# Performance work log

Hardware: AMD Instinct MI355X
Metric: run time of the kernel (lower is better)

The kernel has to match this reference:

```python
import jax, jax.numpy as jnp
import numpy as np

B, M, K, L, E = 1024, 16, 32, 50, 64
NUM_ACT, NUM_USER = 100000, 500000
AVG_M = float(M)  # avg group size; equals M since groups are batched to fixed size


def setup_inputs() -> dict:
    key = jax.random.key(0)
    ks = jax.random.split(key, 24)
    s = 1.0 / np.sqrt(E)
    u = lambda k, shape: jax.random.uniform(k, shape, minval=-s, maxval=s, dtype=jnp.float32)
    return {
        "members": jax.random.randint(ks[0], (B, M), 0, NUM_USER),
        "neighbors": jax.random.randint(ks[1], (B, M, K), 0, NUM_USER),
        "act_inputs": jax.random.randint(ks[2], (B,), 0, NUM_ACT),
        "act_seqs": jax.random.randint(ks[3], (B, M, L), 0, NUM_ACT),
        "act_table": jax.random.normal(ks[4], (NUM_ACT, E), dtype=jnp.float32) * 0.02,
        "user_table": jax.random.normal(ks[5], (NUM_USER, E), dtype=jnp.float32) * 0.02,
        "W_ih": u(ks[6], (4 * E, E)),
        "W_hh": u(ks[7], (4 * E, E)),
        "b_ih": u(ks[8], (4 * E,)),
        "b_hh": u(ks[9], (4 * E,)),
        "gcn_W": u(ks[10], (E, E)),
        "gcn_b": u(ks[11], (E,)),
        "pna_W1": u(ks[12], (4 * E, E)),
        "pna_b1": u(ks[13], (E,)),
        "pna_W2": u(ks[14], (E, E)),
        "pna_b2": u(ks[15], (E,)),
        "pna_W3": u(ks[16], (E, E)),
        "pna_b3": u(ks[17], (E,)),
        "pred_W1": u(ks[18], (3 * E, 8)),
        "pred_b1": u(ks[19], (8,)),
        "pred_W2": u(ks[20], (8, 1)),
        "pred_b2": u(ks[21], (1,)),
    }


def _lstm_last(x, W_ih, W_hh, b):
    # x: [N, L, E]; returns last hidden state [N, E] (PyTorch gate order i,f,g,o)
    n = x.shape[0]
    h0 = jnp.zeros((n, E), x.dtype)

    def step(carry, xt):
        h, c = carry
        gates = xt @ W_ih.T + h @ W_hh.T + b  # [N, 4E]
        i, f, g, o = jnp.split(gates, 4, axis=-1)
        c = jax.nn.sigmoid(f) * c + jax.nn.sigmoid(i) * jnp.tanh(g)
        h = jax.nn.sigmoid(o) * jnp.tanh(c)
        return (h, c), None

    (h, _), _ = jax.lax.scan(step, (h0, h0), jnp.swapaxes(x, 0, 1))
    return h


def reference(members, neighbors, act_inputs, act_seqs, act_table, user_table,
              W_ih, W_hh, b_ih, b_hh, gcn_W, gcn_b,
              pna_W1, pna_b1, pna_W2, pna_b2, pna_W3, pna_b3,
              pred_W1, pred_b1, pred_W2, pred_b2):
    act_e = act_table[act_inputs]  # [B, E] target activity embeddings
    # per-member LSTM encoding of activity sequences, batched over all B*M members
    seq_e = act_table[act_seqs].reshape(B * M, L, E)
    m_act = _lstm_last(seq_e, W_ih, W_hh, b_ih + b_hh).reshape(B, M, E)
    # GCN: mean over {member} U neighbors, then linear + relu
    mem_e = user_table[members]                     # [B, M, E]
    nbr_sum = user_table[neighbors].sum(axis=2)     # [B, M, E]
    agg = (mem_e + nbr_sum) / (K + 1)
    m_gcn = jax.nn.relu(agg @ gcn_W.T + gcn_b)      # [B, M, E]
    fus = m_act + m_gcn                             # [B, M, E]
    # PNA-style set aggregation: {mean,max} x {identity, amplification}
    mean = fus.mean(axis=1)
    mx = fus.max(axis=1)
    amp = jnp.log(M + 1.0) / jnp.log(AVG_M + 1.0)
    feats = jnp.concatenate([mean, mx, mean * amp, mx * amp], axis=-1)  # [B, 4E]
    h = jax.nn.relu(feats @ pna_W1 + pna_b1)
    h = jax.nn.relu(h @ pna_W2 + pna_b2)
    grp = h @ pna_W3 + pna_b3                        # [B, E]
    # predict layer
    cat = jnp.concatenate([grp * act_e, grp, act_e], axis=-1)  # [B, 3E]
    hh = jax.nn.relu(cat @ pred_W1 + pred_b1)
    y = jax.nn.sigmoid(hh @ pred_W2 + pred_b2)       # [B, 1]
    return y
```

## Files before the change

kernel.cpp:

```cpp
#include <hip/hip_runtime.h>
#include <hip/hip_bf16.h>
#include <math.h>

#define BB   1024
#define MM   16
#define KK   32
#define LL   50
#define EE   64
#define NACT 100000

typedef __attribute__((ext_vector_type(8))) short short8;
typedef float v4f __attribute__((ext_vector_type(4)));

__device__ __forceinline__ float rcpf(float x) { return __builtin_amdgcn_rcpf(x); }
__device__ __forceinline__ float exp2_fast(float x) {
    float r;
    asm("v_exp_f32 %0, %1" : "=v"(r) : "v"(x));
    return r;
}

__device__ __forceinline__ unsigned cvt_pk_bf16(float lo, float hi) {
    unsigned r;
    asm("v_cvt_pk_bf16_f32 %0, %1, %2" : "=v"(r) : "v"(lo), "v"(hi));
    return r;
}

__device__ __forceinline__ void block_sync_lds() {
    __builtin_amdgcn_sched_barrier(0);
    asm volatile("s_waitcnt lgkmcnt(0)" ::: "memory");
    __builtin_amdgcn_s_barrier();
    __builtin_amdgcn_sched_barrier(0);
}

__global__ __launch_bounds__(256)
void cvt_table(const float* __restrict__ src, unsigned* __restrict__ dst)
{
    const int i = blockIdx.x * 256 + threadIdx.x;
    if (i < (NACT * EE) / 8) {
        const float4* s = reinterpret_cast<const float4*>(src) + (size_t)i * 2;
        float4 a = s[0], b = s[1];
        uint4 o;
        o.x = cvt_pk_bf16(a.x, a.y);
        o.y = cvt_pk_bf16(a.z, a.w);
        o.z = cvt_pk_bf16(b.x, b.y);
        o.w = cvt_pk_bf16(b.z, b.w);
        reinterpret_cast<uint4*>(dst)[i] = o;
    }
}

__global__ __launch_bounds__(256, 2)
void lstm_fused(const int* __restrict__ act_seqs, const unsigned short* __restrict__ act_bf,
                const int* __restrict__ members, const int* __restrict__ neighbors,
                const float* __restrict__ user_table,
                const float* __restrict__ W_ih, const float* __restrict__ W_hh,
                const float* __restrict__ b_ih, const float* __restrict__ b_hh,
                const int* __restrict__ act_inputs, const float* __restrict__ act_table,
                const float* __restrict__ gcn_W, const float* __restrict__ gcn_b,
                const float* __restrict__ pna_W1, const float* __restrict__ pna_b1,
                const float* __restrict__ pna_W2, const float* __restrict__ pna_b2,
                const float* __restrict__ pna_W3, const float* __restrict__ pna_b3,
                const float* __restrict__ pred_W1, const float* __restrict__ pred_b1,
                const float* __restrict__ pred_W2, const float* __restrict__ pred_b2,
                float* __restrict__ out)
{
    __shared__ __align__(16) short sH[4][1024];
    __shared__ int sIdx[32 * LL];
    __shared__ int sNbr[32 * 33];
    __shared__ float sFus[32][64];
    __shared__ float sAgg[32][64];
    __shared__ float sWg[64][66];
    __shared__ float sF[2][256];
    __shared__ float sP[2][2][64];
    __shared__ float sH1[2][64];
    __shared__ float sH2[2][64];
    __shared__ float sGrp[2][64];
    __shared__ float sActe[2][64];
    __shared__ float sHH[2][8];

    const int t    = threadIdx.x;
    const int blk  = blockIdx.x;
    const int lane = t & 63;
    const int w    = t >> 6;
    const int lr   = lane & 15;
    const int lb   = lane >> 4;

    for (int i = t; i < 32 * LL; i += 256) sIdx[i] = act_seqs[blk * (32 * LL) + i];
    for (int i = t; i < 32 * 33; i += 256) {
        const int p = i / 33, j = i - p * 33;
        const int base = blk * 32 + p;
        sNbr[i] = (j == 0) ? members[base] : neighbors[base * KK + j - 1];
    }

    const float L2E = 1.44269504088896f;
    float gscale[4];
    gscale[0] = -L2E; gscale[1] = -L2E; gscale[2] = 2.0f * L2E; gscale[3] = -L2E;

    short8 Bf[2][4][2];
    #pragma unroll
    for (int mat = 0; mat < 2; ++mat) {
        const float* W = mat ? W_hh : W_ih;
        #pragma unroll
        for (int g = 0; g < 4; ++g) {
            const int j = g * 64 + w * 16 + lr;
            const float sc = gscale[g];
            #pragma unroll
            for (int ks = 0; ks < 2; ++ks) {
                const float4* p = reinterpret_cast<const float4*>(&W[(size_t)j * 64 + ks * 32 + lb * 8]);
                float4 v0 = p[0], v1 = p[1];
                uint4 o;
                o.x = cvt_pk_bf16(sc * v0.x, sc * v0.y);
                o.y = cvt_pk_bf16(sc * v0.z, sc * v0.w);
                o.z = cvt_pk_bf16(sc * v1.x, sc * v1.y);
                o.w = cvt_pk_bf16(sc * v1.z, sc * v1.w);
                Bf[mat][g][ks] = __builtin_bit_cast(short8, o);
            }
        }
    }
    float bias[4];
    #pragma unroll
    for (int g = 0; g < 4; ++g) {
        const int j = g * 64 + w * 16 + lr;
        bias[g] = gscale[g] * (b_ih[j] + b_hh[j]);
    }

    float hA[4], cA[4], hB[4], cB[4];
    #pragma unroll
    for (int r = 0; r < 4; ++r) { hA[r] = 0.0f; cA[r] = 0.0f; hB[r] = 0.0f; cB[r] = 0.0f; }

    reinterpret_cast<uint4*>(sH)[t] = make_uint4(0u, 0u, 0u, 0u);
    __syncthreads();

    const int gpair = t >> 3;
    const int gec   = t & 7;
    const float* gut = user_table + (size_t)gec * 8;
    float gacc[8];
    #pragma unroll
    for (int q = 0; q < 8; ++q) gacc[q] = 0.0f;
    float4 gld0, gld1;
    {
        const int gi = sNbr[gpair * 33 + 0];
        const float4* gp = reinterpret_cast<const float4*>(gut + (size_t)gi * EE);
        gld0 = gp[0]; gld1 = gp[1];
    }

    const char* tbl8 = reinterpret_cast<const char*>(act_bf) + lb * 16;
    const int ibA = lr * LL;
    const int ibB = (16 + lr) * LL;

    int idA = sIdx[ibA + 0], idB = sIdx[ibB + 0];
    short8 axA0 = *reinterpret_cast<const short8*>(tbl8 + (size_t)idA * 128);
    short8 axA1 = *reinterpret_cast<const short8*>(tbl8 + (size_t)idA * 128 + 64);
    short8 axB0 = *reinterpret_cast<const short8*>(tbl8 + (size_t)idB * 128);
    short8 axB1 = *reinterpret_cast<const short8*>(tbl8 + (size_t)idB * 128 + 64);
    idA = sIdx[ibA + 1]; idB = sIdx[ibB + 1];

    const int offA0 = lr * 128 + ((lb ^ (lr & 7)) << 4);
    const int offA1 = lr * 128 + (((lb + 4) ^ (lr & 7)) << 4);
    int hw_off[4];
    #pragma unroll
    for (int r = 0; r < 4; ++r) {
        const int s = lb * 4 + r, e = w * 16 + lr;
        hw_off[r] = s * 128 + ((((e >> 3) ^ (s & 7)) << 4)) + (e & 7) * 2;
    }
    char* const sHb = reinterpret_cast<char*>(sH);

    #pragma unroll 2
    for (int step = 0; step < LL; ++step) {
        const int cb  = (step & 1) << 12;
        const int nb_ = cb ^ 4096;

        if (step < 33) {
            gacc[0] += gld0.x; gacc[1] += gld0.y; gacc[2] += gld0.z; gacc[3] += gld0.w;
            gacc[4] += gld1.x; gacc[5] += gld1.y; gacc[6] += gld1.z; gacc[7] += gld1.w;
            if (step < 32) {
                const int gi = sNbr[gpair * 33 + step + 1];
                const float4* gp = reinterpret_cast<const float4*>(gut + (size_t)gi * EE);
                gld0 = gp[0]; gld1 = gp[1];
            }
        }

        short8 nxA0 = *reinterpret_cast<const short8*>(tbl8 + (size_t)idA * 128);
        short8 nxA1 = *reinterpret_cast<const short8*>(tbl8 + (size_t)idA * 128 + 64);
        short8 nxB0 = *reinterpret_cast<const short8*>(tbl8 + (size_t)idB * 128);
        short8 nxB1 = *reinterpret_cast<const short8*>(tbl8 + (size_t)idB * 128 + 64);
        {
            const int s2 = (step + 2 < LL) ? (step + 2) : (LL - 1);
            idA = sIdx[ibA + s2]; idB = sIdx[ibB + s2];
        }

        short8 ahA0 = *reinterpret_cast<const short8*>(sHb + cb + offA0);
        short8 ahA1 = *reinterpret_cast<const short8*>(sHb + cb + offA1);
        short8 ahB0 = *reinterpret_cast<const short8*>(sHb + cb + 2048 + offA0);
        short8 ahB1 = *reinterpret_cast<const short8*>(sHb + cb + 2048 + offA1);

        v4f accA[4], accB[4];
        #pragma unroll
        for (int g = 0; g < 4; ++g) {
            v4f a; a[0] = bias[g]; a[1] = bias[g]; a[2] = bias[g]; a[3] = bias[g];
            accA[g] = a; accB[g] = a;
        }
        #pragma unroll
        for (int g = 0; g < 4; ++g) {
            accA[g] = __builtin_amdgcn_mfma_f32_16x16x32_bf16(axA0, Bf[0][g][0], accA[g], 0, 0, 0);
            accA[g] = __builtin_amdgcn_mfma_f32_16x16x32_bf16(axA1, Bf[0][g][1], accA[g], 0, 0, 0);
            accA[g] = __builtin_amdgcn_mfma_f32_16x16x32_bf16(ahA0, Bf[1][g][0], accA[g], 0, 0, 0);
            accA[g] = __builtin_amdgcn_mfma_f32_16x16x32_bf16(ahA1, Bf[1][g][1], accA[g], 0, 0, 0);
        }
        #pragma unroll
        for (int g = 0; g < 4; ++g) {
            accB[g] = __builtin_amdgcn_mfma_f32_16x16x32_bf16(axB0, Bf[0][g][0], accB[g], 0, 0, 0);
            accB[g] = __builtin_amdgcn_mfma_f32_16x16x32_bf16(axB1, Bf[0][g][1], accB[g], 0, 0, 0);
            accB[g] = __builtin_amdgcn_mfma_f32_16x16x32_bf16(ahB0, Bf[1][g][0], accB[g], 0, 0, 0);
            accB[g] = __builtin_amdgcn_mfma_f32_16x16x32_bf16(ahB1, Bf[1][g][1], accB[g], 0, 0, 0);
        }

        {
            char* SH = sHb + nb_;
            #pragma unroll
            for (int r = 0; r < 4; ++r) {
                const float si = rcpf(1.0f + exp2_fast(accA[0][r]));
                const float sf = rcpf(1.0f + exp2_fast(accA[1][r]));
                const float tg = fmaf(-2.0f, rcpf(1.0f + exp2_fast(accA[2][r])), 1.0f);
                const float so = rcpf(1.0f + exp2_fast(accA[3][r]));
                const float cc = fmaf(sf, cA[r], si * tg);
                cA[r] = cc;
                hA[r] = so * fmaf(-2.0f, rcpf(1.0f + exp2_fast(cc * (2.0f * L2E))), 1.0f);
            }
            const unsigned a01 = cvt_pk_bf16(hA[0], hA[1]);
            const unsigned a23 = cvt_pk_bf16(hA[2], hA[3]);
            *reinterpret_cast<short*>(SH + hw_off[0]) = (short)(a01 & 0xFFFF);
            *reinterpret_cast<short*>(SH + hw_off[1]) = (short)(a01 >> 16);
            *reinterpret_cast<short*>(SH + hw_off[2]) = (short)(a23 & 0xFFFF);
            *reinterpret_cast<short*>(SH + hw_off[3]) = (short)(a23 >> 16);
            SH += 2048;
            #pragma unroll
            for (int r = 0; r < 4; ++r) {
                const float si = rcpf(1.0f + exp2_fast(accB[0][r]));
                const float sf = rcpf(1.0f + exp2_fast(accB[1][r]));
                const float tg = fmaf(-2.0f, rcpf(1.0f + exp2_fast(accB[2][r])), 1.0f);
                const float so = rcpf(1.0f + exp2_fast(accB[3][r]));
                const float cc = fmaf(sf, cB[r], si * tg);
                cB[r] = cc;
                hB[r] = so * fmaf(-2.0f, rcpf(1.0f + exp2_fast(cc * (2.0f * L2E))), 1.0f);
            }
            const unsigned b01 = cvt_pk_bf16(hB[0], hB[1]);
            const unsigned b23 = cvt_pk_bf16(hB[2], hB[3]);
            *reinterpret_cast<short*>(SH + hw_off[0]) = (short)(b01 & 0xFFFF);
            *reinterpret_cast<short*>(SH + hw_off[1]) = (short)(b01 >> 16);
            *reinterpret_cast<short*>(SH + hw_off[2]) = (short)(b23 & 0xFFFF);
            *reinterpret_cast<short*>(SH + hw_off[3]) = (short)(b23 >> 16);
        }

        block_sync_lds();

        axA0 = nxA0; axA1 = nxA1; axB0 = nxB0; axB1 = nxB1;
    }


    #pragma unroll
    for (int r = 0; r < 4; ++r) {
        sFus[lb * 4 + r][w * 16 + lr]      = hA[r];
        sFus[16 + lb * 4 + r][w * 16 + lr] = hB[r];
    }
    {
        const float sc = 1.0f / 33.0f;
        float* ar = &sAgg[gpair][gec * 8];
        #pragma unroll
        for (int q = 0; q < 8; ++q) ar[q] = gacc[q] * sc;
    }
    {
        const int row = t >> 2, cq = (t & 3) * 16;
        #pragma unroll
        for (int i = 0; i < 4; ++i) {
            float4 v = *reinterpret_cast<const float4*>(&gcn_W[row * 64 + cq + i * 4]);
            sWg[row][cq + i * 4 + 0] = v.x;
            sWg[row][cq + i * 4 + 1] = v.y;
            sWg[row][cq + i * 4 + 2] = v.z;
            sWg[row][cq + i * 4 + 3] = v.w;
        }
    }
    if (t < 128) {
        const int q = t >> 6, e = t & 63;
        sActe[q][e] = act_table[(size_t)act_inputs[blk * 2 + q] * EE + e];
    }
    __syncthreads();

    {
        const int m = t >> 3, e0 = (t & 7) * 8;
        float acc[8];
        #pragma unroll
        for (int i = 0; i < 8; ++i) acc[i] = gcn_b[e0 + i];
        for (int k = 0; k < 64; ++k) {
            const float a = sAgg[m][k];
            #pragma unroll
            for (int i = 0; i < 8; ++i) acc[i] = fmaf(a, sWg[e0 + i][k], acc[i]);
        }
        #pragma unroll
        for (int i = 0; i < 8; ++i) sFus[m][e0 + i] += fmaxf(acc[i], 0.0f);
    }
    __syncthreads();

    if (t < 128) {
        const int q = t >> 6, e = t & 63;
        float mn = 0.0f, mx = -INFINITY;
        #pragma unroll
        for (int m = 0; m < MM; ++m) { float v = sFus[q * 16 + m][e]; mn += v; mx = fmaxf(mx, v); }
        mn *= (1.0f / 16.0f);
        sF[q][e] = mn; sF[q][64 + e] = mx; sF[q][128 + e] = mn; sF[q][192 + e] = mx;
    }
    __syncthreads();

    {
        const int q = t >> 7, kh = (t >> 6) & 1, j = t & 63;
        float p = 0.0f;
        const float* Wp = pna_W1 + (size_t)(kh * 128) * 64 + j;
        const float* fp = &sF[q][kh * 128];
        #pragma unroll 8
        for (int k = 0; k < 128; ++k) p = fmaf(fp[k], Wp[(size_t)k * 64], p);
        sP[q][kh][j] = p;
    }
    __syncthreads();
    if (t < 128) {
        const int q = t >> 6, j = t & 63;
        sH1[q][j] = fmaxf(pna_b1[j] + sP[q][0][j] + sP[q][1][j], 0.0f);
    }
    __syncthreads();

    if (t < 128) {
        const int q = t >> 6, j = t & 63;
        float p = 0.0f;
        #pragma unroll 8
        for (int k = 0; k < 64; ++k) p = fmaf(sH1[q][k], pna_W2[(size_t)k * 64 + j], p);
        sH2[q][j] = fmaxf(pna_b2[j] + p, 0.0f);
    }
    __syncthreads();

    if (t < 128) {
        const int q = t >> 6, j = t & 63;
        float p = 0.0f;
        #pragma unroll 8
        for (int k = 0; k < 64; ++k) p = fmaf(sH2[q][k], pna_W3[(size_t)k * 64 + j], p);
        sGrp[q][j] = pna_b3[j] + p;
    }
    __syncthreads();

    if (t < 16) {
        const int q = t >> 3, j = t & 7;
        float a = pred_b1[j];
        for (int k = 0; k < 192; ++k) {
            float cv = (k < 64) ? sGrp[q][k] * sActe[q][k]
                                : ((k < 128) ? sGrp[q][k - 64] : sActe[q][k - 128]);
            a = fmaf(cv, pred_W1[k * 8 + j], a);
        }
        sHH[q][j] = fmaxf(a, 0.0f);
    }
    __syncthreads();
    if (t < 2) {
        float y = pred_b2[0];
        #pragma unroll
        for (int jj = 0; jj < 8; ++jj) y = fmaf(sHH[t][jj], pred_W2[jj], y);
        out[blk * 2 + t] = 1.0f / (1.0f + expf(-y));
    }
}

extern "C" void kernel_launch(void* const* d_in, const int* in_sizes, int n_in,
                              void* d_out, int out_size, void* d_ws, size_t ws_size,
                              hipStream_t stream) {
    const int*   members    = (const int*)d_in[0];
    const int*   neighbors  = (const int*)d_in[1];
    const int*   act_inputs = (const int*)d_in[2];
    const int*   act_seqs   = (const int*)d_in[3];
    const float* act_table  = (const float*)d_in[4];
    const float* user_table = (const float*)d_in[5];
    const float* W_ih       = (const float*)d_in[6];
    const float* W_hh       = (const float*)d_in[7];
    const float* b_ih       = (const float*)d_in[8];
    const float* b_hh       = (const float*)d_in[9];
    const float* gcn_W      = (const float*)d_in[10];
    const float* gcn_b      = (const float*)d_in[11];
    const float* pna_W1     = (const float*)d_in[12];
    const float* pna_b1     = (const float*)d_in[13];
    const float* pna_W2     = (const float*)d_in[14];
    const float* pna_b2     = (const float*)d_in[15];
    const float* pna_W3     = (const float*)d_in[16];
    const float* pna_b3     = (const float*)d_in[17];
    const float* pred_W1    = (const float*)d_in[18];
    const float* pred_b1    = (const float*)d_in[19];
    const float* pred_W2    = (const float*)d_in[20];
    const float* pred_b2    = (const float*)d_in[21];

    unsigned short* act_bf = (unsigned short*)d_ws;

    cvt_table<<<dim3((NACT * EE / 8 + 255) / 256), dim3(256), 0, stream>>>(
        act_table, (unsigned*)act_bf);

    lstm_fused<<<dim3(512), dim3(256), 0, stream>>>(
        act_seqs, act_bf, members, neighbors, user_table,
        W_ih, W_hh, b_ih, b_hh,
        act_inputs, act_table,
        gcn_W, gcn_b, pna_W1, pna_b1, pna_W2, pna_b2, pna_W3, pna_b3,
        pred_W1, pred_b1, pred_W2, pred_b2, (float*)d_out);
}
```

Before: 124.4 us.

## Compute GCN linear with MFMA and split tail matvecs across more threads

Replaces the scalar LDS-based GCN matmul with bf16 MFMA, using gcn_W fragments preloaded in registers and the aggregated neighbor sums staged in the existing swizzled LDS buffer. This removes the sWg/sAgg shared arrays and fuses the ReLU and LSTM add into the fragment writeback. The pna_W2/W3 and pred_W1 matvecs are split over all 256 threads with partial-sum reductions, and the act_e gather moves to the prologue. It adds bf16 rounding to the GCN input and weights, plus extra barriers and register pressure.

```diff
diff --git a/kernel.cpp b/kernel.cpp
--- a/kernel.cpp
+++ b/kernel.cpp
@@ -66,11 +66,10 @@
     __shared__ __align__(16) short sH[4][1024];
     __shared__ int sIdx[32 * LL];
     __shared__ int sNbr[32 * 33];
-    __shared__ float sFus[32][64];
-    __shared__ float sAgg[32][64];
-    __shared__ float sWg[64][66];
+    __shared__ float sFus[32][66];
     __shared__ float sF[2][256];
     __shared__ float sP[2][2][64];
+    __shared__ float sP7[2][8][8];
     __shared__ float sH1[2][64];
     __shared__ float sH2[2][64];
     __shared__ float sGrp[2][64];
@@ -89,6 +88,10 @@
         const int p = i / 33, j = i - p * 33;
         const int base = blk * 32 + p;
         sNbr[i] = (j == 0) ? members[base] : neighbors[base * KK + j - 1];
+    }
+    if (t < 128) {
+        const int q = t >> 6, e = t & 63;
+        sActe[q][e] = act_table[(size_t)act_inputs[blk * 2 + q] * EE + e];
     }
 
     const float L2E = 1.44269504088896f;
@@ -116,6 +119,21 @@
             }
         }
     }
+    short8 Bg[2];
+    #pragma unroll
+    for (int ks = 0; ks < 2; ++ks) {
+        const int j = w * 16 + lr;
+        const float4* p = reinterpret_cast<const float4*>(&gcn_W[(size_t)j * 64 + ks * 32 + lb * 8]);
+        float4 v0 = p[0], v1 = p[1];
+        uint4 o;
+        o.x = cvt_pk_bf16(v0.x, v0.y);
+        o.y = cvt_pk_bf16(v0.z, v0.w);
+        o.z = cvt_pk_bf16(v1.x, v1.y);
+        o.w = cvt_pk_bf16(v1.z, v1.w);
+        Bg[ks] = __builtin_bit_cast(short8, o);
+    }
+    const float gb = gcn_b[w * 16 + lr];
+
     float bias[4];
     #pragma unroll
     for (int g = 0; g < 4; ++g) {
@@ -257,46 +275,35 @@
     }
 
 
-    #pragma unroll
-    for (int r = 0; r < 4; ++r) {
-        sFus[lb * 4 + r][w * 16 + lr]      = hA[r];
-        sFus[16 + lb * 4 + r][w * 16 + lr] = hB[r];
-    }
     {
         const float sc = 1.0f / 33.0f;
-        float* ar = &sAgg[gpair][gec * 8];
-        #pragma unroll
-        for (int q = 0; q < 8; ++q) ar[q] = gacc[q] * sc;
-    }
-    {
-        const int row = t >> 2, cq = (t & 3) * 16;
-        #pragma unroll
-        for (int i = 0; i < 4; ++i) {
-            float4 v = *reinterpret_cast<const float4*>(&gcn_W[row * 64 + cq + i * 4]);
-            sWg[row][cq + i * 4 + 0] = v.x;
-            sWg[row][cq + i * 4 + 1] = v.y;
-            sWg[row][cq + i * 4 + 2] = v.z;
-            sWg[row][cq + i * 4 + 3] = v.w;
-        }
-    }
-    if (t < 128) {
-        const int q = t >> 6, e = t & 63;
-        sActe[q][e] = act_table[(size_t)act_inputs[blk * 2 + q] * EE + e];
-    }
-    __syncthreads();
-
-    {
-        const int m = t >> 3, e0 = (t & 7) * 8;
-        float acc[8];
-        #pragma unroll
-        for (int i = 0; i < 8; ++i) acc[i] = gcn_b[e0 + i];
-        for (int k = 0; k < 64; ++k) {
-            const float a = sAgg[m][k];
-            #pragma unroll
-            for (int i = 0; i < 8; ++i) acc[i] = fmaf(a, sWg[e0 + i][k], acc[i]);
-        }
-        #pragma unroll
-        for (int i = 0; i < 8; ++i) sFus[m][e0 + i] += fmaxf(acc[i], 0.0f);
+        uint4 pk;
+        pk.x = cvt_pk_bf16(gacc[0] * sc, gacc[1] * sc);
+        pk.y = cvt_pk_bf16(gacc[2] * sc, gacc[3] * sc);
+        pk.z = cvt_pk_bf16(gacc[4] * sc, gacc[5] * sc);
+        pk.w = cvt_pk_bf16(gacc[6] * sc, gacc[7] * sc);
+        const int row = gpair & 15;
+        const int off = ((gpair >> 4) << 11) + row * 128 + ((gec ^ (row & 7)) << 4);
+        *reinterpret_cast<uint4*>(sHb + off) = pk;
+    }
+    __syncthreads();
+
+    {
+        short8 agA0 = *reinterpret_cast<const short8*>(sHb + offA0);
+        short8 agA1 = *reinterpret_cast<const short8*>(sHb + offA1);
+        short8 agB0 = *reinterpret_cast<const short8*>(sHb + 2048 + offA0);
+        short8 agB1 = *reinterpret_cast<const short8*>(sHb + 2048 + offA1);
+        v4f z4 = {0.0f, 0.0f, 0.0f, 0.0f};
+        v4f gA = __builtin_amdgcn_mfma_f32_16x16x32_bf16(agA0, Bg[0], z4, 0, 0, 0);
+        gA = __builtin_amdgcn_mfma_f32_16x16x32_bf16(agA1, Bg[1], gA, 0, 0, 0);
+        v4f gB = __builtin_amdgcn_mfma_f32_16x16x32_bf16(agB0, Bg[0], z4, 0, 0, 0);
+        gB = __builtin_amdgcn_mfma_f32_16x16x32_bf16(agB1, Bg[1], gB, 0, 0, 0);
+        const int e = w * 16 + lr;
+        #pragma unroll
+        for (int r = 0; r < 4; ++r) {
+            sFus[lb * 4 + r][e]      = hA[r] + fmaxf(gA[r] + gb, 0.0f);
+            sFus[16 + lb * 4 + r][e] = hB[r] + fmaxf(gB[r] + gb, 0.0f);
+        }
     }
     __syncthreads();
 
@@ -315,7 +322,7 @@
         float p = 0.0f;
         const float* Wp = pna_W1 + (size_t)(kh * 128) * 64 + j;
         const float* fp = &sF[q][kh * 128];
-        #pragma unroll 8
+        #pragma unroll 16
         for (int k = 0; k < 128; ++k) p = fmaf(fp[k], Wp[(size_t)k * 64], p);
         sP[q][kh][j] = p;
     }
@@ -326,32 +333,54 @@
     }
     __syncthreads();
 
+    {
+        const int q = t >> 7, kh = (t >> 6) & 1, j = t & 63;
+        float p = 0.0f;
+        #pragma unroll
+        for (int k = 0; k < 32; ++k)
+            p = fmaf(sH1[q][kh * 32 + k], pna_W2[(size_t)(kh * 32 + k) * 64 + j], p);
+        sP[q][kh][j] = p;
+    }
+    __syncthreads();
     if (t < 128) {
         const int q = t >> 6, j = t & 63;
+        sH2[q][j] = fmaxf(pna_b2[j] + sP[q][0][j] + sP[q][1][j], 0.0f);
+    }
+    __syncthreads();
+
+    {
+        const int q = t >> 7, kh = (t >> 6) & 1, j = t & 63;
         float p = 0.0f;
-        #pragma unroll 8
-        for (int k = 0; k < 64; ++k) p = fmaf(sH1[q][k], pna_W2[(size_t)k * 64 + j], p);
-        sH2[q][j] = fmaxf(pna_b2[j] + p, 0.0f);
-    }
-    __syncthreads();
-
+        #pragma unroll
+        for (int k = 0; k < 32; ++k)
+            p = fmaf(sH2[q][kh * 32 + k], pna_W3[(size_t)(kh * 32 + k) * 64 + j], p);
+        sP[q][kh][j] = p;
+    }
+    __syncthreads();
     if (t < 128) {
         const int q = t >> 6, j = t & 63;
-        float p = 0.0f;
-        #pragma unroll 8
-        for (int k = 0; k < 64; ++k) p = fmaf(sH2[q][k], pna_W3[(size_t)k * 64 + j], p);
-        sGrp[q][j] = pna_b3[j] + p;
-    }
-    __syncthreads();
-
+        sGrp[q][j] = pna_b3[j] + sP[q][0][j] + sP[q][1][j];
+    }
+    __syncthreads();
+
+    if (t < 128) {
+        const int q = t >> 6, kg = (t >> 3) & 7, j = t & 7;
+        float a = 0.0f;
+        #pragma unroll
+        for (int kk = 0; kk < 24; ++kk) {
+            const int k = kg * 24 + kk;
+            const float cv = (k < 64) ? sGrp[q][k] * sActe[q][k]
+                                      : ((k < 128) ? sGrp[q][k - 64] : sActe[q][k - 128]);
+            a = fmaf(cv, pred_W1[k * 8 + j], a);
+        }
+        sP7[q][kg][j] = a;
+    }
+    __syncthreads();
     if (t < 16) {
         const int q = t >> 3, j = t & 7;
         float a = pred_b1[j];
-        for (int k = 0; k < 192; ++k) {
-            float cv = (k < 64) ? sGrp[q][k] * sActe[q][k]
-                                : ((k < 128) ? sGrp[q][k - 64] : sActe[q][k - 128]);
-            a = fmaf(cv, pred_W1[k * 8 + j], a);
-        }
+        #pragma unroll
+        for (int kg = 0; kg < 8; ++kg) a += sP7[q][kg][j];
         sHH[q][j] = fmaxf(a, 0.0f);
     }
     __syncthreads();
```

New measurement: 106.0 us. -14.8%, faster.
